# Kernel tuning notes

Hardware: AMD Instinct MI355X
Metric: run time of the kernel (lower is better)

The kernel has to match this reference:

```python
import jax, jax.numpy as jnp
import numpy as np

MAX_DISP = 48
PATCH = 3
OFFSET = 0
PAD = PATCH // 2
EPS = 1e-3


def _unfold(x, P, pad):
    # x: [B,C,H,W] -> [B,C,K2,H,W], K2 enumerated row-major over the PxP window
    B, C, H, W = x.shape
    xp = jnp.pad(x, ((0, 0), (0, 0), (pad, pad), (pad, pad)))
    return jnp.stack([xp[:, :, i:i + H, j:j + W]
                      for i in range(P) for j in range(P)], axis=2)


def _normalize(x, axes):
    # torch F.normalize: x / clamp(||x||_2, min=eps)
    n = jnp.sqrt(jnp.sum(x * x, axis=axes, keepdims=True))
    return x / jnp.maximum(n, EPS)


def setup_inputs() -> dict:
    key = jax.random.key(0)
    k1, k2, k3 = jax.random.split(key, 3)
    shp = (2, 32, 128, 416)
    return {
        "xl": jax.random.normal(k1, shp, dtype=jnp.float32),
        "xm": jax.random.normal(k2, shp, dtype=jnp.float32),
        "xr": jax.random.normal(k3, shp, dtype=jnp.float32),
    }


def reference(xl, xm, xr):
    B, C, H, W = xl.shape
    K2 = PATCH * PATCH
    scale = (C * K2) ** 0.5

    pl = _normalize(_unfold(xl, PATCH, PAD), (1, 2))  # [B,C,K2,H,W]
    pr = _normalize(_unfold(xr, PATCH, PAD), (1, 2))
    fl = _normalize(xm, (1,))                          # [B,C,H,W]

    # fl is constant over the K2 axis, so sum patches over K2 once for sim_L/sim_R
    Sl = pl.sum(axis=2)  # [B,C,H,W]
    Sr = pr.sum(axis=2)

    cL, cR, cLR = [], [], []
    for d in range(OFFSET, OFFSET + MAX_DISP):
        if d > 0:
            # shifted_l[w] = patches_l[w+d] (zero right pad); shifted_r[w] = patches_r[w-d]
            sL = jnp.einsum('bchw,bchw->bhw', fl[..., :W - d], Sl[..., d:])
            sL = jnp.pad(sL, ((0, 0), (0, 0), (0, d)))
            sR = jnp.einsum('bchw,bchw->bhw', fl[..., d:], Sr[..., :W - d])
            sR = jnp.pad(sR, ((0, 0), (0, 0), (d, 0)))
            wlr = W - 2 * d  # overlap region of the two opposite shifts
            if wlr > 0:
                sLR = jnp.einsum('bckhw,bckhw->bhw', pl[..., 2 * d:], pr[..., :wlr])
                sLR = jnp.pad(sLR, ((0, 0), (0, 0), (d, d)))
            else:
                sLR = jnp.zeros((B, H, W), xl.dtype)
        else:
            sL = jnp.einsum('bchw,bchw->bhw', fl, Sl)
            sR = jnp.einsum('bchw,bchw->bhw', fl, Sr)
            sLR = jnp.einsum('bckhw,bckhw->bhw', pl, pr)
        cL.append(sL / scale)
        cR.append(sR / scale)
        cLR.append(sLR / scale)

    cost = jnp.stack([jnp.stack(cL, 1), jnp.stack(cR, 1), jnp.stack(cLR, 1)], axis=1)
    return jnp.clip(cost, -10.0, 10.0).astype(jnp.float16)  # [B,3,D,H,W]
```

## Files before the change

kernel.cpp:

```cpp
#include <hip/hip_runtime.h>
#include <math.h>

#define B 2
#define C 32
#define H 128
#define W 416
#define D 48
#define HW (H*W)
#define CHW (C*HW)
#define EPSN 1e-3f
#define ISCALE 0.05892556509887896f
#define LSTR 36
#define DSPL (D / 2)

__device__ __forceinline__ float clip10(float x) {
    return fminf(fmaxf(x, -10.0f), 10.0f);
}

__global__ __launch_bounds__(256) void k_sq(const float* __restrict__ xl,
                                            const float* __restrict__ xr,
                                            const float* __restrict__ xm,
                                            float* __restrict__ sql,
                                            float* __restrict__ sqr,
                                            float* __restrict__ inm) {
    int idx = blockIdx.x * 256 + threadIdx.x;
    if (idx >= B * HW) return;
    int b = idx / HW, hw = idx - b * HW;
    const float* pl = xl + (size_t)b * CHW + hw;
    const float* pr = xr + (size_t)b * CHW + hw;
    const float* pm = xm + (size_t)b * CHW + hw;
    float al = 0.f, ar = 0.f, am = 0.f;
#pragma unroll
    for (int c = 0; c < C; ++c) {
        float vl = pl[c * HW], vr = pr[c * HW], vm = pm[c * HW];
        al += vl * vl; ar += vr * vr; am += vm * vm;
    }
    sql[idx] = al;
    sqr[idx] = ar;
    inm[idx] = 1.0f / fmaxf(sqrtf(am), EPSN);
}

__global__ __launch_bounds__(256) void k_norm(const float* __restrict__ sql,
                                              const float* __restrict__ sqr,
                                              float* __restrict__ inl,
                                              float* __restrict__ inr) {
    int idx = blockIdx.x * 256 + threadIdx.x;
    if (idx >= B * HW) return;
    int b = idx / HW, hw = idx - b * HW;
    int h = hw / W, w = hw - h * W;
    float sl = 0.f, sr = 0.f;
#pragma unroll
    for (int di = -1; di <= 1; ++di) {
        int hh = h + di;
        if (hh < 0 || hh >= H) continue;
#pragma unroll
        for (int dj = -1; dj <= 1; ++dj) {
            int ww = w + dj;
            if (ww < 0 || ww >= W) continue;
            int p = b * HW + hh * W + ww;
            sl += sql[p];
            sr += sqr[p];
        }
    }
    inl[idx] = 1.0f / fmaxf(sqrtf(sl), EPSN);
    inr[idx] = 1.0f / fmaxf(sqrtf(sr), EPSN);
}

__global__ __launch_bounds__(256) void k_box(const float* __restrict__ xl,
                                             const float* __restrict__ xr,
                                             float* __restrict__ boxl,
                                             float* __restrict__ boxr) {
    int idx = blockIdx.x * 256 + threadIdx.x;
    int w4 = (idx % (W / 4)) * 4;
    int h = (idx / (W / 4)) % H;
    int rest = idx / (H * (W / 4));
    size_t base = (size_t)rest * HW;
    float4 al = {0.f, 0.f, 0.f, 0.f}, ar = {0.f, 0.f, 0.f, 0.f};
#pragma unroll
    for (int dh = -1; dh <= 1; ++dh) {
        int hh = h + dh;
        if (hh < 0 || hh >= H) continue;
        const float* rl = xl + base + hh * W;
        const float* rr = xr + base + hh * W;
        float4 m = *(const float4*)(rl + w4);
        float lm = (w4 > 0) ? rl[w4 - 1] : 0.f;
        float rm = (w4 + 4 < W) ? rl[w4 + 4] : 0.f;
        al.x += lm + m.x + m.y;  al.y += m.x + m.y + m.z;
        al.z += m.y + m.z + m.w; al.w += m.z + m.w + rm;
        float4 n = *(const float4*)(rr + w4);
        float ln = (w4 > 0) ? rr[w4 - 1] : 0.f;
        float rn = (w4 + 4 < W) ? rr[w4 + 4] : 0.f;
        ar.x += ln + n.x + n.y;  ar.y += n.x + n.y + n.z;
        ar.z += n.y + n.z + n.w; ar.w += n.z + n.w + rn;
    }
    *(float4*)(boxl + base + h * W + w4) = al;
    *(float4*)(boxr + base + h * W + w4) = ar;
}

__device__ __forceinline__ void stage_row_v2(const float* __restrict__ gsrc,
                                             float* __restrict__ lds,
                                             int tid, int nthreads) {
    for (int t = tid; t < (W / 4) * C; t += nthreads) {
        int rw = t & 7;
        int cl = (t >> 3) & 7;
        int g  = t >> 6;
        int wg = g % 13;
        int ch = g / 13;
        int c  = ch * 8 + cl;
        int w4 = (wg * 8 + rw) * 4;
        float4 v = *(const float4*)(gsrc + (size_t)c * HW + w4);
        lds[(w4 + 0) * LSTR + c] = v.x;
        lds[(w4 + 1) * LSTR + c] = v.y;
        lds[(w4 + 2) * LSTR + c] = v.z;
        lds[(w4 + 3) * LSTR + c] = v.w;
    }
}

__device__ __forceinline__ float dot32(const float* __restrict__ fl,
                                       const float* __restrict__ col) {
    const float4* c4 = (const float4*)col;
    float a = 0.0f;
#pragma unroll
    for (int q = 0; q < 8; ++q) {
        float4 v = c4[q];
        a += fl[4 * q + 0] * v.x + fl[4 * q + 1] * v.y
           + fl[4 * q + 2] * v.z + fl[4 * q + 3] * v.w;
    }
    return a;
}

__device__ __forceinline__ void dot32x2(const float* __restrict__ fl0,
                                        const float* __restrict__ fl1,
                                        const float* __restrict__ col,
                                        float& a0, float& a1) {
    const float4* c4 = (const float4*)col;
    float s0 = 0.f, s1 = 0.f;
#pragma unroll
    for (int q = 0; q < 8; ++q) {
        float4 v = c4[q];
        s0 += fl0[4 * q + 0] * v.x + fl0[4 * q + 1] * v.y
            + fl0[4 * q + 2] * v.z + fl0[4 * q + 3] * v.w;
        s1 += fl1[4 * q + 0] * v.x + fl1[4 * q + 1] * v.y
            + fl1[4 * q + 2] * v.z + fl1[4 * q + 3] * v.w;
    }
    a0 = s0; a1 = s1;
}

__global__ __launch_bounds__(256) void k_lr(const float* __restrict__ xm,
                                            const float* __restrict__ boxl,
                                            const float* __restrict__ boxr,
                                            const float* __restrict__ inl,
                                            const float* __restrict__ inr,
                                            const float* __restrict__ inm,
                                            float* __restrict__ out) {
    __shared__ float sB[W * LSTR];
    __shared__ float sIn[W];
    int tid = threadIdx.x;
    int h = blockIdx.x;
    int b = blockIdx.y;
    int d0 = blockIdx.z * DSPL;
    bool act = tid < (W / 2);
    int w = 2 * tid;
    int bhw = b * HW + h * W;
    const float* pm = xm + (size_t)b * CHW + h * W;

    float fl0[C], fl1[C];
    if (act) {
        float2 im = *(const float2*)(inm + bhw + w);
#pragma unroll
        for (int c = 0; c < C; ++c) {
            float2 mv = *(const float2*)(pm + c * HW + w);
            fl0[c] = mv.x * im.x;
            fl1[c] = mv.y * im.y;
        }
    } else {
#pragma unroll
        for (int c = 0; c < C; ++c) { fl0[c] = 0.f; fl1[c] = 0.f; }
    }

    stage_row_v2(boxl + (size_t)b * CHW + h * W, sB, tid, 256);
    for (int j = tid; j < W; j += 256) sIn[j] = inl[bhw + j];
    __syncthreads();
    if (act) {
        float* o = out + ((size_t)b * 3 + 0) * D * HW + h * W;
        float a0p = 0.f;
#pragma unroll 4
        for (int j = 0; j <= DSPL; ++j) {
            int v = w + d0 + j;
            float a0 = 0.f, a1 = 0.f;
            if (v < W) {
                dot32x2(fl0, fl1, sB + v * LSTR, a0, a1);
                float s = sIn[v] * ISCALE;
                a0 = clip10(a0 * s);
                a1 = clip10(a1 * s);
            }
            if (j >= 1) {
                int d = d0 + j - 1;
                *(float2*)(o + (size_t)d * HW + w) = make_float2(a0p, a1);
            }
            a0p = a0;
        }
    }
    __syncthreads();

    stage_row_v2(boxr + (size_t)b * CHW + h * W, sB, tid, 256);
    for (int j = tid; j < W; j += 256) sIn[j] = inr[bhw + j];
    __syncthreads();
    if (act) {
        float* o = out + ((size_t)b * 3 + 1) * D * HW + h * W;
        float a0p = 0.f;
#pragma unroll 4
        for (int j = 0; j <= DSPL; ++j) {
            int v = w - d0 - (DSPL - 1) + j;
            float a0 = 0.f, a1 = 0.f;
            if (v >= 0) {
                dot32x2(fl0, fl1, sB + v * LSTR, a0, a1);
                float s = sIn[v] * ISCALE;
                a0 = clip10(a0 * s);
                a1 = clip10(a1 * s);
            }
            if (j >= 1) {
                int d = d0 + DSPL - j;
                *(float2*)(o + (size_t)d * HW + w) = make_float2(a0p, a1);
            }
            a0p = a0;
        }
    }
}

__global__ __launch_bounds__(448) void k_e(const float* __restrict__ xl,
                                           const float* __restrict__ xr,
                                           float* __restrict__ EH) {
    __shared__ float sXL[W * LSTR];
    int tid = threadIdx.x;
    int h = blockIdx.x;
    int b = blockIdx.y;
    int d0 = blockIdx.z * DSPL;
    int lane = tid & 63;
    int wv = tid >> 6;
    int v = wv * 62 + lane - 1;
    bool vin = (v >= 0) && (v < W);
    const float* br = xr + (size_t)b * CHW + h * W;

    float xrv[C];
#pragma unroll
    for (int c = 0; c < C; ++c) xrv[c] = vin ? br[c * HW + v] : 0.0f;

    stage_row_v2(xl + (size_t)b * CHW + h * W, sXL, tid, 448);
    __syncthreads();

    bool wr = (lane >= 1) && (lane <= 62) && (v < W);
    float* pe = EH + (((size_t)b * D) * H + h) * W + v;
    for (int d = d0; d < d0 + DSPL; ++d) {
        int s = 2 * d;
        float e = 0.0f;
        if (vin && v + s < W) e = dot32(xrv, sXL + (v + s) * LSTR);
        float em = __shfl_up(e, 1);
        float ep = __shfl_down(e, 1);
        float eh = em + e + ep;
        if (wr) pe[(size_t)d * HW] = eh;
    }
}

#define DCH 12
__global__ __launch_bounds__(448) void k_lr2(const float* __restrict__ EH,
                                             const float* __restrict__ inl,
                                             const float* __restrict__ inr,
                                             float* __restrict__ out) {
    int w = threadIdx.x;
    int dc = blockIdx.x;
    int h = blockIdx.y;
    int b = blockIdx.z;
    if (w >= W) return;
    int bhw = b * HW + h * W;
    bool hm = (h > 0), hp = (h < H - 1);

    float* o = out + ((size_t)b * 3 + 2) * D * HW + h * W + w;
#pragma unroll
    for (int i = 0; i < DCH; ++i) {
        int d = dc * DCH + i;
        float r = 0.0f;
        if (w >= d && w + d < W) {
            int vc = w - d;
            const float* base = EH + ((size_t)b * D + d) * HW + vc;
            float e = base[h * W];
            if (hm) e += base[(h - 1) * W];
            if (hp) e += base[(h + 1) * W];
            float nl = inl[bhw + w + d];
            float nr = inr[bhw + vc];
            r = clip10(e * nl * nr * ISCALE);
        }
        o[(size_t)d * HW] = r;
    }
}

extern "C" void kernel_launch(void* const* d_in, const int* in_sizes, int n_in,
                              void* d_out, int out_size, void* d_ws, size_t ws_size,
                              hipStream_t stream) {
    const float* xl = (const float*)d_in[0];
    const float* xm = (const float*)d_in[1];
    const float* xr = (const float*)d_in[2];
    float* out = (float*)d_out;

    float* ws = (float*)d_ws;
    float* boxl = ws;
    float* boxr = boxl + (size_t)B * CHW;
    float* inl  = boxr + (size_t)B * CHW;
    float* inr  = inl + B * HW;
    float* inm  = inr + B * HW;
    float* sql  = inm + B * HW;
    float* sqr  = sql + B * HW;
    float* EH   = sqr + B * HW;

    k_sq<<<dim3((B * HW + 255) / 256), dim3(256), 0, stream>>>(xl, xr, xm, sql, sqr, inm);
    k_norm<<<dim3((B * HW + 255) / 256), dim3(256), 0, stream>>>(sql, sqr, inl, inr);
    k_box<<<dim3((B * CHW / 4 + 255) / 256), dim3(256), 0, stream>>>(xl, xr, boxl, boxr);
    k_e<<<dim3(H, B, 2), dim3(448), 0, stream>>>(xl, xr, EH);
    k_lr<<<dim3(H, B, 2), dim3(256), 0, stream>>>(xm, boxl, boxr, inl, inr, inm, out);
    k_lr2<<<dim3(4, H, B), dim3(448), 0, stream>>>(EH, inl, inr, out);
}
```

Baseline: 193.1 us.

## Use fp16 LDS tiles and fdot2 for correlation dot products, split disparity into four

Box-filtered patches and staged xl rows are now kept in fp16, with LDS rows packed at stride 40 halves, and the 32-channel dot products use packed fp16 dot2 instructions with fp32 accumulation. This halves LDS footprint and global traffic for the box buffers and halves the dot-product instruction count. The disparity range is now split into four blocks per row instead of two, which raises parallelism but restages the LDS row twice as often. fp16 rounding of normalized features and box sums adds precision error.

```diff
diff --git a/kernel.cpp b/kernel.cpp
--- a/kernel.cpp
+++ b/kernel.cpp
@@ -10,8 +10,22 @@
 #define CHW (C*HW)
 #define EPSN 1e-3f
 #define ISCALE 0.05892556509887896f
-#define LSTR 36
-#define DSPL (D / 2)
+#define LSTRH 40
+#define NDSP 4
+#define DSPL (D / NDSP)
+
+typedef _Float16 half2v __attribute__((ext_vector_type(2)));
+typedef _Float16 half4v __attribute__((ext_vector_type(4)));
+typedef _Float16 half8v __attribute__((ext_vector_type(8)));
+
+#if defined(__has_builtin)
+#if __has_builtin(__builtin_amdgcn_fdot2)
+#define FDOT2(a, b, c) __builtin_amdgcn_fdot2((a), (b), (c), false)
+#endif
+#endif
+#ifndef FDOT2
+#define FDOT2(a, b, c) ((c) + (float)(a)[0] * (float)(b)[0] + (float)(a)[1] * (float)(b)[1])
+#endif
 
 __device__ __forceinline__ float clip10(float x) {
     return fminf(fmaxf(x, -10.0f), 10.0f);
@@ -68,8 +82,8 @@
 
 __global__ __launch_bounds__(256) void k_box(const float* __restrict__ xl,
                                              const float* __restrict__ xr,
-                                             float* __restrict__ boxl,
-                                             float* __restrict__ boxr) {
+                                             _Float16* __restrict__ boxl,
+                                             _Float16* __restrict__ boxr) {
     int idx = blockIdx.x * 256 + threadIdx.x;
     int w4 = (idx % (W / 4)) * 4;
     int h = (idx / (W / 4)) % H;
@@ -93,13 +107,34 @@
         ar.x += ln + n.x + n.y;  ar.y += n.x + n.y + n.z;
         ar.z += n.y + n.z + n.w; ar.w += n.z + n.w + rn;
     }
-    *(float4*)(boxl + base + h * W + w4) = al;
-    *(float4*)(boxr + base + h * W + w4) = ar;
-}
-
-__device__ __forceinline__ void stage_row_v2(const float* __restrict__ gsrc,
-                                             float* __restrict__ lds,
-                                             int tid, int nthreads) {
+    half4v ol = {(_Float16)al.x, (_Float16)al.y, (_Float16)al.z, (_Float16)al.w};
+    half4v orr = {(_Float16)ar.x, (_Float16)ar.y, (_Float16)ar.z, (_Float16)ar.w};
+    *(half4v*)(boxl + base + h * W + w4) = ol;
+    *(half4v*)(boxr + base + h * W + w4) = orr;
+}
+
+__device__ __forceinline__ void stage_row_h(const _Float16* __restrict__ gsrc,
+                                            _Float16* __restrict__ lds,
+                                            int tid, int nthreads) {
+    for (int t = tid; t < (W / 4) * C; t += nthreads) {
+        int rw = t & 7;
+        int cl = (t >> 3) & 7;
+        int g  = t >> 6;
+        int wg = g % 13;
+        int ch = g / 13;
+        int c  = ch * 8 + cl;
+        int w4 = (wg * 8 + rw) * 4;
+        half4v v = *(const half4v*)(gsrc + (size_t)c * HW + w4);
+        lds[(w4 + 0) * LSTRH + c] = v[0];
+        lds[(w4 + 1) * LSTRH + c] = v[1];
+        lds[(w4 + 2) * LSTRH + c] = v[2];
+        lds[(w4 + 3) * LSTRH + c] = v[3];
+    }
+}
+
+__device__ __forceinline__ void stage_row_cvt(const float* __restrict__ gsrc,
+                                              _Float16* __restrict__ lds,
+                                              int tid, int nthreads) {
     for (int t = tid; t < (W / 4) * C; t += nthreads) {
         int rw = t & 7;
         int cl = (t >> 3) & 7;
@@ -109,51 +144,56 @@
         int c  = ch * 8 + cl;
         int w4 = (wg * 8 + rw) * 4;
         float4 v = *(const float4*)(gsrc + (size_t)c * HW + w4);
-        lds[(w4 + 0) * LSTR + c] = v.x;
-        lds[(w4 + 1) * LSTR + c] = v.y;
-        lds[(w4 + 2) * LSTR + c] = v.z;
-        lds[(w4 + 3) * LSTR + c] = v.w;
-    }
-}
-
-__device__ __forceinline__ float dot32(const float* __restrict__ fl,
-                                       const float* __restrict__ col) {
-    const float4* c4 = (const float4*)col;
-    float a = 0.0f;
-#pragma unroll
-    for (int q = 0; q < 8; ++q) {
-        float4 v = c4[q];
-        a += fl[4 * q + 0] * v.x + fl[4 * q + 1] * v.y
-           + fl[4 * q + 2] * v.z + fl[4 * q + 3] * v.w;
-    }
-    return a;
-}
-
-__device__ __forceinline__ void dot32x2(const float* __restrict__ fl0,
-                                        const float* __restrict__ fl1,
-                                        const float* __restrict__ col,
-                                        float& a0, float& a1) {
-    const float4* c4 = (const float4*)col;
+        lds[(w4 + 0) * LSTRH + c] = (_Float16)v.x;
+        lds[(w4 + 1) * LSTRH + c] = (_Float16)v.y;
+        lds[(w4 + 2) * LSTRH + c] = (_Float16)v.z;
+        lds[(w4 + 3) * LSTRH + c] = (_Float16)v.w;
+    }
+}
+
+__device__ __forceinline__ float dot16(const half2v* __restrict__ a,
+                                       const _Float16* __restrict__ col) {
+    const half8v* c8 = (const half8v*)col;
+    float s = 0.f;
+#pragma unroll
+    for (int q = 0; q < 4; ++q) {
+        half8v v = c8[q];
+#pragma unroll
+        for (int i = 0; i < 4; ++i) {
+            half2v p = {v[2 * i], v[2 * i + 1]};
+            s = FDOT2(a[4 * q + i], p, s);
+        }
+    }
+    return s;
+}
+
+__device__ __forceinline__ void dot16x2(const half2v* __restrict__ a0,
+                                        const half2v* __restrict__ a1,
+                                        const _Float16* __restrict__ col,
+                                        float& r0, float& r1) {
+    const half8v* c8 = (const half8v*)col;
     float s0 = 0.f, s1 = 0.f;
 #pragma unroll
-    for (int q = 0; q < 8; ++q) {
-        float4 v = c4[q];
-        s0 += fl0[4 * q + 0] * v.x + fl0[4 * q + 1] * v.y
-            + fl0[4 * q + 2] * v.z + fl0[4 * q + 3] * v.w;
-        s1 += fl1[4 * q + 0] * v.x + fl1[4 * q + 1] * v.y
-            + fl1[4 * q + 2] * v.z + fl1[4 * q + 3] * v.w;
-    }
-    a0 = s0; a1 = s1;
+    for (int q = 0; q < 4; ++q) {
+        half8v v = c8[q];
+#pragma unroll
+        for (int i = 0; i < 4; ++i) {
+            half2v p = {v[2 * i], v[2 * i + 1]};
+            s0 = FDOT2(a0[4 * q + i], p, s0);
+            s1 = FDOT2(a1[4 * q + i], p, s1);
+        }
+    }
+    r0 = s0; r1 = s1;
 }
 
 __global__ __launch_bounds__(256) void k_lr(const float* __restrict__ xm,
-                                            const float* __restrict__ boxl,
-                                            const float* __restrict__ boxr,
+                                            const _Float16* __restrict__ boxl,
+                                            const _Float16* __restrict__ boxr,
                                             const float* __restrict__ inl,
                                             const float* __restrict__ inr,
                                             const float* __restrict__ inm,
                                             float* __restrict__ out) {
-    __shared__ float sB[W * LSTR];
+    __shared__ _Float16 sB[W * LSTRH];
     __shared__ float sIn[W];
     int tid = threadIdx.x;
     int h = blockIdx.x;
@@ -164,21 +204,26 @@
     int bhw = b * HW + h * W;
     const float* pm = xm + (size_t)b * CHW + h * W;
 
-    float fl0[C], fl1[C];
+    half2v fl0[C / 2], fl1[C / 2];
     if (act) {
         float2 im = *(const float2*)(inm + bhw + w);
 #pragma unroll
-        for (int c = 0; c < C; ++c) {
-            float2 mv = *(const float2*)(pm + c * HW + w);
-            fl0[c] = mv.x * im.x;
-            fl1[c] = mv.y * im.y;
+        for (int c2 = 0; c2 < C / 2; ++c2) {
+            float2 ma = *(const float2*)(pm + (2 * c2) * HW + w);
+            float2 mb = *(const float2*)(pm + (2 * c2 + 1) * HW + w);
+            half2v f0 = {(_Float16)(ma.x * im.x), (_Float16)(mb.x * im.x)};
+            half2v f1 = {(_Float16)(ma.y * im.y), (_Float16)(mb.y * im.y)};
+            fl0[c2] = f0; fl1[c2] = f1;
         }
     } else {
 #pragma unroll
-        for (int c = 0; c < C; ++c) { fl0[c] = 0.f; fl1[c] = 0.f; }
-    }
-
-    stage_row_v2(boxl + (size_t)b * CHW + h * W, sB, tid, 256);
+        for (int c2 = 0; c2 < C / 2; ++c2) {
+            half2v z = {(_Float16)0.f, (_Float16)0.f};
+            fl0[c2] = z; fl1[c2] = z;
+        }
+    }
+
+    stage_row_h(boxl + (size_t)b * CHW + h * W, sB, tid, 256);
     for (int j = tid; j < W; j += 256) sIn[j] = inl[bhw + j];
     __syncthreads();
     if (act) {
@@ -189,7 +234,7 @@
             int v = w + d0 + j;
             float a0 = 0.f, a1 = 0.f;
             if (v < W) {
-                dot32x2(fl0, fl1, sB + v * LSTR, a0, a1);
+                dot16x2(fl0, fl1, sB + v * LSTRH, a0, a1);
                 float s = sIn[v] * ISCALE;
                 a0 = clip10(a0 * s);
                 a1 = clip10(a1 * s);
@@ -203,7 +248,7 @@
     }
     __syncthreads();
 
-    stage_row_v2(boxr + (size_t)b * CHW + h * W, sB, tid, 256);
+    stage_row_h(boxr + (size_t)b * CHW + h * W, sB, tid, 256);
     for (int j = tid; j < W; j += 256) sIn[j] = inr[bhw + j];
     __syncthreads();
     if (act) {
@@ -214,7 +259,7 @@
             int v = w - d0 - (DSPL - 1) + j;
             float a0 = 0.f, a1 = 0.f;
             if (v >= 0) {
-                dot32x2(fl0, fl1, sB + v * LSTR, a0, a1);
+                dot16x2(fl0, fl1, sB + v * LSTRH, a0, a1);
                 float s = sIn[v] * ISCALE;
                 a0 = clip10(a0 * s);
                 a1 = clip10(a1 * s);
@@ -231,7 +276,7 @@
 __global__ __launch_bounds__(448) void k_e(const float* __restrict__ xl,
                                            const float* __restrict__ xr,
                                            float* __restrict__ EH) {
-    __shared__ float sXL[W * LSTR];
+    __shared__ _Float16 sXL[W * LSTRH];
     int tid = threadIdx.x;
     int h = blockIdx.x;
     int b = blockIdx.y;
@@ -242,11 +287,16 @@
     bool vin = (v >= 0) && (v < W);
     const float* br = xr + (size_t)b * CHW + h * W;
 
-    float xrv[C];
-#pragma unroll
-    for (int c = 0; c < C; ++c) xrv[c] = vin ? br[c * HW + v] : 0.0f;
-
-    stage_row_v2(xl + (size_t)b * CHW + h * W, sXL, tid, 448);
+    half2v xrv[C / 2];
+#pragma unroll
+    for (int c2 = 0; c2 < C / 2; ++c2) {
+        float va = vin ? br[(2 * c2) * HW + v] : 0.f;
+        float vb = vin ? br[(2 * c2 + 1) * HW + v] : 0.f;
+        half2v x = {(_Float16)va, (_Float16)vb};
+        xrv[c2] = x;
+    }
+
+    stage_row_cvt(xl + (size_t)b * CHW + h * W, sXL, tid, 448);
     __syncthreads();
 
     bool wr = (lane >= 1) && (lane <= 62) && (v < W);
@@ -254,7 +304,7 @@
     for (int d = d0; d < d0 + DSPL; ++d) {
         int s = 2 * d;
         float e = 0.0f;
-        if (vin && v + s < W) e = dot32(xrv, sXL + (v + s) * LSTR);
+        if (vin && v + s < W) e = dot16(xrv, sXL + (v + s) * LSTRH);
         float em = __shfl_up(e, 1);
         float ep = __shfl_down(e, 1);
         float eh = em + e + ep;
@@ -303,19 +353,19 @@
     float* out = (float*)d_out;
 
     float* ws = (float*)d_ws;
-    float* boxl = ws;
-    float* boxr = boxl + (size_t)B * CHW;
-    float* inl  = boxr + (size_t)B * CHW;
+    float* EH   = ws;
+    float* inl  = EH + (size_t)B * D * HW;
     float* inr  = inl + B * HW;
     float* inm  = inr + B * HW;
     float* sql  = inm + B * HW;
     float* sqr  = sql + B * HW;
-    float* EH   = sqr + B * HW;
+    _Float16* boxl = (_Float16*)(sqr + B * HW);
+    _Float16* boxr = boxl + (size_t)B * CHW;
 
     k_sq<<<dim3((B * HW + 255) / 256), dim3(256), 0, stream>>>(xl, xr, xm, sql, sqr, inm);
     k_norm<<<dim3((B * HW + 255) / 256), dim3(256), 0, stream>>>(sql, sqr, inl, inr);
     k_box<<<dim3((B * CHW / 4 + 255) / 256), dim3(256), 0, stream>>>(xl, xr, boxl, boxr);
-    k_e<<<dim3(H, B, 2), dim3(448), 0, stream>>>(xl, xr, EH);
-    k_lr<<<dim3(H, B, 2), dim3(256), 0, stream>>>(xm, boxl, boxr, inl, inr, inm, out);
+    k_e<<<dim3(H, B, NDSP), dim3(448), 0, stream>>>(xl, xr, EH);
+    k_lr<<<dim3(H, B, NDSP), dim3(256), 0, stream>>>(xm, boxl, boxr, inl, inr, inm, out);
     k_lr2<<<dim3(4, H, B), dim3(448), 0, stream>>>(EH, inl, inr, out);
 }
```

Result: no change. 196.6 us (+1.8%).
